# Kernel tuning notes

Measured on AMD Instinct MI355X. Metric: run time of the kernel, lower is better.

Reference implementation:

```python
import jax, jax.numpy as jnp
import numpy as np

B, S, H = 2, 2048, 256
NS, NR = 512, 512
FFN_RATIO = 4


def setup_inputs() -> dict:
    key = jax.random.key(0)
    ks = jax.random.split(key, 8)
    token_reps = jax.random.normal(ks[0], (B, S, H), dtype=jnp.float32)
    token_masks = jnp.ones((B, S), dtype=bool)
    span_reps = jax.random.normal(ks[1], (B, NS, H), dtype=jnp.float32)
    # spans: start in [0, S-16), length in [1, 16) -> valid [start, end) windows
    starts = jax.random.randint(ks[2], (B, NS), 0, S - 16)
    lens = jax.random.randint(ks[3], (B, NS), 1, 16)
    span_ids = jnp.stack([starts, starts + lens], axis=-1)  # (B, NS, 2)
    rel_ids = jax.random.randint(ks[4], (B, NR, 2), 0, NS)  # (B, NR, 2)
    rel_masks = jnp.ones((B, NR), dtype=bool)
    neg_limit = jnp.float32(-6.0e4)
    d_in = 3 * H
    d_ff = FFN_RATIO * d_in
    W1 = jax.random.normal(ks[5], (d_in, d_ff), dtype=jnp.float32) / np.float32(np.sqrt(d_in))
    b1 = jnp.zeros((d_ff,), dtype=jnp.float32)
    W2 = jax.random.normal(ks[6], (d_ff, H), dtype=jnp.float32) / np.float32(np.sqrt(d_ff))
    b2 = jnp.zeros((H,), dtype=jnp.float32)
    return {
        "token_reps": token_reps, "token_masks": token_masks,
        "span_reps": span_reps, "span_ids": span_ids,
        "rel_ids": rel_ids, "rel_masks": rel_masks, "neg_limit": neg_limit,
        "W1": W1, "b1": b1, "W2": W2, "b2": b2,
    }


def reference(token_reps, token_masks, span_reps, span_ids, rel_ids, rel_masks,
              neg_limit, W1, b1, W2, b2):
    seq_len = token_reps.shape[1]
    head_ids = rel_ids[..., 0]  # (B, NR)
    tail_ids = rel_ids[..., 1]
    # gather head/tail span reps: (B, NR, H)
    head_reps = jnp.take_along_axis(span_reps, head_ids[..., None], axis=1)
    tail_reps = jnp.take_along_axis(span_reps, tail_ids[..., None], axis=1)
    # span boundaries per relation: (B, NR)
    head_start = jnp.take_along_axis(span_ids[..., 0], head_ids, axis=1)
    head_end = jnp.take_along_axis(span_ids[..., 1], head_ids, axis=1)
    tail_start = jnp.take_along_axis(span_ids[..., 0], tail_ids, axis=1)
    tail_end = jnp.take_along_axis(span_ids[..., 1], tail_ids, axis=1)
    seq = jnp.arange(seq_len)[None, None, :]  # (1, 1, S)
    head_m = (seq >= head_start[..., None]) & (seq < head_end[..., None])
    tail_m = (seq >= tail_start[..., None]) & (seq < tail_end[..., None])
    # 'between' base context: tokens strictly between the two spans
    lo = jnp.minimum(head_end, tail_end)[..., None]
    hi = jnp.maximum(head_start, tail_start)[..., None]
    base = (seq >= lo) & (seq < hi)
    ctx_mask = base & ~(head_m | tail_m) & rel_masks[..., None] & token_masks[:, None, :]  # (B, NR, S)
    # masked max-pool over seq: (B, NR, S, H) -> (B, NR, H)
    masked = jnp.where(ctx_mask[..., None], token_reps[:, None, :, :], neg_limit)
    context_reps = jnp.max(masked, axis=2)
    # no-context fallback: fully-masked relations -> zero vector
    all_masked = jnp.all(context_reps == neg_limit, axis=-1)
    context_reps = jnp.where(all_masked[..., None], jnp.float32(0.0), context_reps)
    rel_reps = jnp.concatenate([head_reps, tail_reps, context_reps], axis=-1)  # (B, NR, 3H)
    h = jax.nn.relu(rel_reps @ W1 + b1)  # dropout = identity at inference
    return h @ W2 + b2
```

## Files before the change

kernel.cpp:

```cpp
#include <hip/hip_runtime.h>
#include <hip/hip_bf16.h>
#include <stdint.h>

#define Bb 2
#define Ss 2048
#define Hh 256
#define NSs 512
#define NRr 512
#define DIN 768
#define DFF 3072
#define Mm (Bb*NRr)
#define KSLICES 4

typedef __attribute__((ext_vector_type(8))) short short8;
typedef __attribute__((ext_vector_type(4))) short short4b;
typedef __attribute__((ext_vector_type(4))) float floatx4;
typedef __attribute__((ext_vector_type(2))) float floatx2;

__device__ __forceinline__ short f2bf(float f) {
  uint32_t u = __float_as_uint(f);
  u += 0x7fffu + ((u >> 16) & 1u);
  return (short)(u >> 16);
}

__device__ __forceinline__ short4b f2bf4(floatx4 v) {
  short4b r;
  r.x = f2bf(v.x); r.y = f2bf(v.y); r.z = f2bf(v.z); r.w = f2bf(v.w);
  return r;
}

__device__ __forceinline__ uint32_t pack_bf2_rne(float lo, float hi) {
  uint32_t ul = __float_as_uint(lo); ul += 0x7fffu + ((ul >> 16) & 1u);
  uint32_t uh = __float_as_uint(hi); uh += 0x7fffu + ((uh >> 16) & 1u);
  return (uh & 0xffff0000u) | (ul >> 16);
}

__device__ __forceinline__ uint32_t max_packed(uint32_t a, uint32_t b) {
  float a0 = __uint_as_float(a << 16), a1 = __uint_as_float(a & 0xffff0000u);
  float b0 = __uint_as_float(b << 16), b1 = __uint_as_float(b & 0xffff0000u);
  float m0 = fmaxf(a0, b0), m1 = fmaxf(a1, b1);
  return (__float_as_uint(m1) & 0xffff0000u) | (__float_as_uint(m0) >> 16);
}

__device__ __forceinline__ void gld_lds16(const void* g, void* l) {
  __builtin_amdgcn_global_load_lds(
      (const __attribute__((address_space(1))) void*)g,
      (__attribute__((address_space(3))) void*)l, 16, 0, 0);
}

__global__ __launch_bounds__(256) void ctx_lds(
    const float* __restrict__ token_reps,
    const int* __restrict__ span_ids,
    const int* __restrict__ rel_ids,
    short* __restrict__ X)
{
  __shared__ uint32_t Lv[8][Ss];
  int t = threadIdx.x;
  int bid = blockIdx.x;
  int b = bid >> 7;
  int r7 = bid & 127;
  int L = ((r7 >> 6) & 1) * 8 + (r7 & 7);
  int m = (r7 >> 3) & 7;
  int g = L * 8 + m;
  int c2 = g * 2;

#pragma unroll
  for (int j = 0; j < 8; ++j) {
    int i = j * 256 + t;
    floatx2 v = *(const floatx2*)&token_reps[((size_t)b * Ss + i) * Hh + c2];
    Lv[0][i] = pack_bf2_rne(v.x, v.y);
  }
  __syncthreads();
#pragma unroll
  for (int k = 1; k <= 7; ++k) {
    int d = 1 << (k - 1);
#pragma unroll
    for (int j = 0; j < 8; ++j) {
      int i = j * 256 + t;
      Lv[k][i] = max_packed(Lv[k - 1][i], Lv[k - 1][min(i + d, Ss - 1)]);
    }
    __syncthreads();
  }

#pragma unroll
  for (int rr = 0; rr < 2; ++rr) {
    int r = rr * 256 + t;
    int hid = rel_ids[(b * NRr + r) * 2 + 0];
    int tid_ = rel_ids[(b * NRr + r) * 2 + 1];
    int hs = span_ids[(b * NSs + hid) * 2 + 0];
    int he = span_ids[(b * NSs + hid) * 2 + 1];
    int ts = span_ids[(b * NSs + tid_) * 2 + 0];
    int te = span_ids[(b * NSs + tid_) * 2 + 1];
    int lo = min(he, te), hi = max(hs, ts);
    int s1 = hs, e1 = he, s2 = ts, e2 = te;
    if (s2 < s1) { s1 = ts; e1 = te; s2 = hs; e2 = he; }

    int ia[3], ibv[3], ni = 0;
    if (e1 >= s2) {
      int me = max(e1, e2);
      int a = lo, bb2 = min(hi, s1); if (a < bb2) { ia[ni]=a; ibv[ni]=bb2; ni++; }
      a = max(lo, me); bb2 = hi;     if (a < bb2) { ia[ni]=a; ibv[ni]=bb2; ni++; }
    } else {
      int a = lo, bb2 = min(hi, s1);      if (a < bb2) { ia[ni]=a; ibv[ni]=bb2; ni++; }
      a = max(lo, e1); bb2 = min(hi, s2); if (a < bb2) { ia[ni]=a; ibv[ni]=bb2; ni++; }
      a = max(lo, e2); bb2 = hi;          if (a < bb2) { ia[ni]=a; ibv[ni]=bb2; ni++; }
    }

    uint32_t acc = 0xff80ff80u;
    for (int q = 0; q < ni; ++q) {
      int a = ia[q], e = ibv[q], len = e - a;
      if (len >= 128) {
        int x = a;
        for (; x + 128 <= e; x += 128) acc = max_packed(acc, Lv[7][x]);
        if (x < e) acc = max_packed(acc, Lv[7][e - 128]);
      } else {
        int k = 31 - __builtin_clz(len);
        acc = max_packed(acc, Lv[k][a]);
        acc = max_packed(acc, Lv[k][e - (1 << k)]);
      }
    }
    if (ni == 0) acc = 0;
    *(uint32_t*)&X[(size_t)(b * NRr + r) * DIN + 2 * Hh + c2] = acc;
  }
}

__global__ __launch_bounds__(256) void gather_and_convT(
    const float* __restrict__ span_reps,
    const int* __restrict__ rel_ids,
    short* __restrict__ X,
    const float* __restrict__ W1, short* __restrict__ W1t,
    const float* __restrict__ W2, short* __restrict__ W2t)
{
  __shared__ float tile[32][33];
  int bid = blockIdx.x;
  int tid = threadIdx.x;

  if (bid < Mm / 4) {
    int w = tid >> 6, lane = tid & 63;
    int br = bid * 4 + w;
    int b = br >> 9, r = br & (NRr - 1);
    int hid = rel_ids[(b * NRr + r) * 2 + 0];
    int tid_ = rel_ids[(b * NRr + r) * 2 + 1];
    int c4 = lane * 4;
    floatx4 hr = *(const floatx4*)&span_reps[((size_t)b * NSs + hid) * Hh + c4];
    floatx4 tr = *(const floatx4*)&span_reps[((size_t)b * NSs + tid_) * Hh + c4];
    size_t base = (size_t)br * DIN;
    *(short4b*)&X[base + c4]      = f2bf4(hr);
    *(short4b*)&X[base + Hh + c4] = f2bf4(tr);
  } else {
    int cb = bid - Mm / 4;
    const float* W; short* Wt; int K, N, bx, by;
    if (cb < 2304) { W = W1; Wt = W1t; K = DIN; N = DFF; bx = cb % 96; by = cb / 96; }
    else { cb -= 2304; W = W2; Wt = W2t; K = DFF; N = Hh; bx = cb % 8; by = cb / 8; }
    int n0 = bx * 32, k0 = by * 32;
    int tx = tid & 31, ty = tid >> 5;
#pragma unroll
    for (int i = 0; i < 4; ++i)
      tile[ty + i * 8][tx] = W[(size_t)(k0 + ty + i * 8) * N + n0 + tx];
    __syncthreads();
#pragma unroll
    for (int i = 0; i < 4; ++i)
      Wt[(size_t)(n0 + ty + i * 8) * K + k0 + tx] = f2bf(tile[tx][ty + i * 8]);
  }
}

__global__ __launch_bounds__(256) void ctx_kernel(
    const float* __restrict__ token_reps,
    const float* __restrict__ span_reps,
    const int* __restrict__ span_ids,
    const int* __restrict__ rel_ids,
    short* __restrict__ X)
{
  int br = blockIdx.x;
  int b = br >> 9;
  int r = br & (NRr - 1);
  int c = threadIdx.x;
  int hid = rel_ids[(b * NRr + r) * 2 + 0];
  int tid = rel_ids[(b * NRr + r) * 2 + 1];
  int hs = span_ids[(b * NSs + hid) * 2 + 0];
  int he = span_ids[(b * NSs + hid) * 2 + 1];
  int ts = span_ids[(b * NSs + tid) * 2 + 0];
  int te = span_ids[(b * NSs + tid) * 2 + 1];
  int lo = min(he, te);
  int hi = max(hs, ts);
  float m = -3.4e38f;
  bool found = false;
  const float* tr = token_reps + ((size_t)b * Ss) * Hh + c;
  for (int s = lo; s < hi; ++s) {
    bool inspan = (s >= hs && s < he) || (s >= ts && s < te);
    if (!inspan) { found = true; m = fmaxf(m, tr[(size_t)s * Hh]); }
  }
  float ctx = found ? m : 0.0f;
  size_t base = (size_t)br * DIN;
  X[base + c]          = f2bf(span_reps[((size_t)b * NSs + hid) * Hh + c]);
  X[base + Hh + c]     = f2bf(span_reps[((size_t)b * NSs + tid) * Hh + c]);
  X[base + 2 * Hh + c] = f2bf(ctx);
}

__global__ void convT(const float* __restrict__ W, short* __restrict__ Wt,
                      int K, int N) {
  __shared__ float tile[32][33];
  int n0 = blockIdx.x * 32, k0 = blockIdx.y * 32;
  int tx = threadIdx.x, ty = threadIdx.y;
#pragma unroll
  for (int i = 0; i < 4; ++i)
    tile[ty + i * 8][tx] = W[(size_t)(k0 + ty + i * 8) * N + n0 + tx];
  __syncthreads();
#pragma unroll
  for (int i = 0; i < 4; ++i)
    Wt[(size_t)(n0 + ty + i * 8) * K + k0 + tx] = f2bf(tile[tx][ty + i * 8]);
}

template <int BM, int BN, bool RELU_BF16>
__global__ __launch_bounds__(256) void gemm_bt(
    const short* __restrict__ A, const short* __restrict__ Bt,
    const float* __restrict__ bias, void* __restrict__ Cout,
    int M, int N, int K) {
  constexpr int BK = 32;
  constexpr int WM = BM / 2, WN = BN / 2;
  constexpr int MT = WM / 16, NT = WN / 16;
  __shared__ __align__(16) short As[BM * BK];
  __shared__ __align__(16) short Bs[BN * BK];

  int tid = threadIdx.x;
  int lane = tid & 63, w = tid >> 6;
  int wi = w & 1, wj = w >> 1;
  int m0 = blockIdx.x * BM, n0 = blockIdx.y * BN;
  int quad = lane >> 4, l16 = lane & 15;

  floatx4 acc[MT][NT];
#pragma unroll
  for (int i = 0; i < MT; ++i)
#pragma unroll
    for (int j = 0; j < NT; ++j)
      acc[i][j] = (floatx4){0.f, 0.f, 0.f, 0.f};

  constexpr int ACH = BM / 16;
  constexpr int BCH = BN / 16;

  for (int kk = 0; kk < K; kk += BK) {
#pragma unroll
    for (int i = 0; i < ACH / 4; ++i) {
      int chunk = w * (ACH / 4) + i;
      int r = chunk * 16 + (lane >> 2);
      gld_lds16(A + (size_t)(m0 + r) * K + kk + (lane & 3) * 8, &As[chunk * 512]);
    }
#pragma unroll
    for (int i = 0; i < BCH / 4; ++i) {
      int chunk = w * (BCH / 4) + i;
      int r = chunk * 16 + (lane >> 2);
      gld_lds16(Bt + (size_t)(n0 + r) * K + kk + (lane & 3) * 8, &Bs[chunk * 512]);
    }
    __syncthreads();

    short8 a[MT], b[NT];
#pragma unroll
    for (int i = 0; i < MT; ++i)
      a[i] = *(const short8*)&As[(wi * WM + i * 16 + l16) * BK + quad * 8];
#pragma unroll
    for (int j = 0; j < NT; ++j)
      b[j] = *(const short8*)&Bs[(wj * WN + j * 16 + l16) * BK + quad * 8];
#pragma unroll
    for (int i = 0; i < MT; ++i)
#pragma unroll
      for (int j = 0; j < NT; ++j)
        acc[i][j] = __builtin_amdgcn_mfma_f32_16x16x32_bf16(a[i], b[j],
                                                            acc[i][j], 0, 0, 0);
    __syncthreads();
  }

#pragma unroll
  for (int i = 0; i < MT; ++i) {
#pragma unroll
    for (int j = 0; j < NT; ++j) {
      int col = n0 + wj * WN + j * 16 + l16;
      float bv = bias[col];
#pragma unroll
      for (int rr = 0; rr < 4; ++rr) {
        int row = m0 + wi * WM + i * 16 + quad * 4 + rr;
        float v = acc[i][j][rr] + bv;
        if (RELU_BF16) {
          v = fmaxf(v, 0.f);
          ((short*)Cout)[(size_t)row * N + col] = f2bf(v);
        } else {
          ((float*)Cout)[(size_t)row * N + col] = v;
        }
      }
    }
  }
}

__global__ __launch_bounds__(256) void gemm_bt_splitk(
    const short* __restrict__ A, const short* __restrict__ Bt,
    float* __restrict__ P, int M, int N, int K) {
  constexpr int BM = 64, BN = 64, BK = 32;
  constexpr int WM = 32, WN = 32;
  constexpr int MT = 2, NT = 2;
  __shared__ __align__(16) short As[BM * BK];
  __shared__ __align__(16) short Bs[BN * BK];

  int tid = threadIdx.x;
  int lane = tid & 63, w = tid >> 6;
  int wi = w & 1, wj = w >> 1;
  int m0 = blockIdx.x * BM, n0 = blockIdx.y * BN;
  int z = blockIdx.z;
  int ksl = K / KSLICES;
  int k_begin = z * ksl, k_end = k_begin + ksl;
  int quad = lane >> 4, l16 = lane & 15;

  floatx4 acc[MT][NT];
#pragma unroll
  for (int i = 0; i < MT; ++i)
#pragma unroll
    for (int j = 0; j < NT; ++j)
      acc[i][j] = (floatx4){0.f, 0.f, 0.f, 0.f};

  for (int kk = k_begin; kk < k_end; kk += BK) {
    {
      int r = w * 16 + (lane >> 2);
      gld_lds16(A + (size_t)(m0 + r) * K + kk + (lane & 3) * 8, &As[w * 512]);
      gld_lds16(Bt + (size_t)(n0 + r) * K + kk + (lane & 3) * 8, &Bs[w * 512]);
    }
    __syncthreads();

    short8 a[MT], b[NT];
#pragma unroll
    for (int i = 0; i < MT; ++i)
      a[i] = *(const short8*)&As[(wi * WM + i * 16 + l16) * BK + quad * 8];
#pragma unroll
    for (int j = 0; j < NT; ++j)
      b[j] = *(const short8*)&Bs[(wj * WN + j * 16 + l16) * BK + quad * 8];
#pragma unroll
    for (int i = 0; i < MT; ++i)
#pragma unroll
      for (int j = 0; j < NT; ++j)
        acc[i][j] = __builtin_amdgcn_mfma_f32_16x16x32_bf16(a[i], b[j],
                                                            acc[i][j], 0, 0, 0);
    __syncthreads();
  }

  float* Pz = P + (size_t)z * M * N;
#pragma unroll
  for (int i = 0; i < MT; ++i)
#pragma unroll
    for (int j = 0; j < NT; ++j) {
      int col = n0 + wj * WN + j * 16 + l16;
#pragma unroll
      for (int rr = 0; rr < 4; ++rr) {
        int row = m0 + wi * WM + i * 16 + quad * 4 + rr;
        Pz[(size_t)row * N + col] = acc[i][j][rr];
      }
    }
}

__global__ __launch_bounds__(256) void splitk_reduce(
    const float* __restrict__ P, const float* __restrict__ bias,
    float* __restrict__ out) {
  int idx = (blockIdx.x * 256 + threadIdx.x) * 4;
  int col = idx & (Hh - 1);
  floatx4 s = *(const floatx4*)&bias[col];
#pragma unroll
  for (int z = 0; z < KSLICES; ++z)
    s += *(const floatx4*)&P[(size_t)z * Mm * Hh + idx];
  *(floatx4*)&out[idx] = s;
}

extern "C" void kernel_launch(void* const* d_in, const int* in_sizes, int n_in,
                              void* d_out, int out_size, void* d_ws,
                              size_t ws_size, hipStream_t stream) {
  const float*   token_reps  = (const float*)d_in[0];
  const float*   span_reps   = (const float*)d_in[2];
  const int*     span_ids    = (const int*)d_in[3];
  const int*     rel_ids     = (const int*)d_in[4];
  const float*   W1 = (const float*)d_in[7];
  const float*   b1 = (const float*)d_in[8];
  const float*   W2 = (const float*)d_in[9];
  const float*   b2 = (const float*)d_in[10];
  float* out = (float*)d_out;

  char* ws = (char*)d_ws;
  short* X    = (short*)ws;
  short* W1t  = X + (size_t)Mm * DIN;
  short* W2t  = W1t + (size_t)DFF * DIN;
  short* hbuf = W2t + (size_t)Hh * DFF;
  size_t bf16_elems = (size_t)Mm * DIN + (size_t)DFF * DIN +
                      (size_t)Hh * DFF + (size_t)Mm * DFF;
  size_t off = (bf16_elems * sizeof(short) + 255) & ~(size_t)255;
  float* Pbuf = (float*)(ws + off);
  size_t need = off + (size_t)KSLICES * Mm * Hh * sizeof(float);

  bool fast = (ws_size >= need);
  if (fast) {
    hipLaunchKernelGGL(ctx_lds, dim3(256), dim3(256), 0, stream,
                       token_reps, span_ids, rel_ids, X);
    hipLaunchKernelGGL(gather_and_convT, dim3(Mm / 4 + 2304 + 768), dim3(256),
                       0, stream, span_reps, rel_ids, X, W1, W1t, W2, W2t);
  } else {
    hipLaunchKernelGGL(ctx_kernel, dim3(Mm), dim3(256), 0, stream,
                       token_reps, span_reps, span_ids, rel_ids, X);
    hipLaunchKernelGGL(convT, dim3(DFF / 32, DIN / 32), dim3(32, 8), 0, stream,
                       W1, W1t, DIN, DFF);
    hipLaunchKernelGGL(convT, dim3(Hh / 32, DFF / 32), dim3(32, 8), 0, stream,
                       W2, W2t, DFF, Hh);
  }
  hipLaunchKernelGGL((gemm_bt<64, 128, true>), dim3(Mm / 64, DFF / 128),
                     dim3(256), 0, stream, X, W1t, b1, (void*)hbuf, Mm, DFF, DIN);
  if (fast) {
    hipLaunchKernelGGL(gemm_bt_splitk, dim3(Mm / 64, Hh / 64, KSLICES),
                       dim3(256), 0, stream, hbuf, W2t, Pbuf, Mm, Hh, DFF);
    hipLaunchKernelGGL(splitk_reduce, dim3(Mm * Hh / 1024), dim3(256), 0,
                       stream, Pbuf, b2, out);
  } else {
    hipLaunchKernelGGL((gemm_bt<64, 64, false>), dim3(Mm / 64, Hh / 64),
                       dim3(256), 0, stream, hbuf, W2t, b2, (void*)out,
                       Mm, Hh, DFF);
  }
}
```

Measured before the change: 123.1 us.

## Merge prep kernels and replace split-K GEMM2 with in-block warp split-K

Result: faster. 118.4 us (-3.8%).

```diff
diff --git a/kernel.cpp b/kernel.cpp
--- a/kernel.cpp
+++ b/kernel.cpp
@@ -10,7 +10,6 @@
 #define DIN 768
 #define DFF 3072
 #define Mm (Bb*NRr)
-#define KSLICES 4
 
 typedef __attribute__((ext_vector_type(8))) short short8;
 typedef __attribute__((ext_vector_type(4))) short short4b;
@@ -48,96 +47,89 @@
       (__attribute__((address_space(3))) void*)l, 16, 0, 0);
 }
 
-__global__ __launch_bounds__(256) void ctx_lds(
+__global__ __launch_bounds__(256) void prep_all(
     const float* __restrict__ token_reps,
+    const float* __restrict__ span_reps,
     const int* __restrict__ span_ids,
-    const int* __restrict__ rel_ids,
-    short* __restrict__ X)
-{
-  __shared__ uint32_t Lv[8][Ss];
-  int t = threadIdx.x;
-  int bid = blockIdx.x;
-  int b = bid >> 7;
-  int r7 = bid & 127;
-  int L = ((r7 >> 6) & 1) * 8 + (r7 & 7);
-  int m = (r7 >> 3) & 7;
-  int g = L * 8 + m;
-  int c2 = g * 2;
-
-#pragma unroll
-  for (int j = 0; j < 8; ++j) {
-    int i = j * 256 + t;
-    floatx2 v = *(const floatx2*)&token_reps[((size_t)b * Ss + i) * Hh + c2];
-    Lv[0][i] = pack_bf2_rne(v.x, v.y);
-  }
-  __syncthreads();
-#pragma unroll
-  for (int k = 1; k <= 7; ++k) {
-    int d = 1 << (k - 1);
-#pragma unroll
-    for (int j = 0; j < 8; ++j) {
-      int i = j * 256 + t;
-      Lv[k][i] = max_packed(Lv[k - 1][i], Lv[k - 1][min(i + d, Ss - 1)]);
-    }
-    __syncthreads();
-  }
-
-#pragma unroll
-  for (int rr = 0; rr < 2; ++rr) {
-    int r = rr * 256 + t;
-    int hid = rel_ids[(b * NRr + r) * 2 + 0];
-    int tid_ = rel_ids[(b * NRr + r) * 2 + 1];
-    int hs = span_ids[(b * NSs + hid) * 2 + 0];
-    int he = span_ids[(b * NSs + hid) * 2 + 1];
-    int ts = span_ids[(b * NSs + tid_) * 2 + 0];
-    int te = span_ids[(b * NSs + tid_) * 2 + 1];
-    int lo = min(he, te), hi = max(hs, ts);
-    int s1 = hs, e1 = he, s2 = ts, e2 = te;
-    if (s2 < s1) { s1 = ts; e1 = te; s2 = hs; e2 = he; }
-
-    int ia[3], ibv[3], ni = 0;
-    if (e1 >= s2) {
-      int me = max(e1, e2);
-      int a = lo, bb2 = min(hi, s1); if (a < bb2) { ia[ni]=a; ibv[ni]=bb2; ni++; }
-      a = max(lo, me); bb2 = hi;     if (a < bb2) { ia[ni]=a; ibv[ni]=bb2; ni++; }
-    } else {
-      int a = lo, bb2 = min(hi, s1);      if (a < bb2) { ia[ni]=a; ibv[ni]=bb2; ni++; }
-      a = max(lo, e1); bb2 = min(hi, s2); if (a < bb2) { ia[ni]=a; ibv[ni]=bb2; ni++; }
-      a = max(lo, e2); bb2 = hi;          if (a < bb2) { ia[ni]=a; ibv[ni]=bb2; ni++; }
-    }
-
-    uint32_t acc = 0xff80ff80u;
-    for (int q = 0; q < ni; ++q) {
-      int a = ia[q], e = ibv[q], len = e - a;
-      if (len >= 128) {
-        int x = a;
-        for (; x + 128 <= e; x += 128) acc = max_packed(acc, Lv[7][x]);
-        if (x < e) acc = max_packed(acc, Lv[7][e - 128]);
-      } else {
-        int k = 31 - __builtin_clz(len);
-        acc = max_packed(acc, Lv[k][a]);
-        acc = max_packed(acc, Lv[k][e - (1 << k)]);
-      }
-    }
-    if (ni == 0) acc = 0;
-    *(uint32_t*)&X[(size_t)(b * NRr + r) * DIN + 2 * Hh + c2] = acc;
-  }
-}
-
-__global__ __launch_bounds__(256) void gather_and_convT(
-    const float* __restrict__ span_reps,
     const int* __restrict__ rel_ids,
     short* __restrict__ X,
     const float* __restrict__ W1, short* __restrict__ W1t,
     const float* __restrict__ W2, short* __restrict__ W2t)
 {
-  __shared__ float tile[32][33];
+  __shared__ __align__(16) uint32_t LvRaw[8 * Ss];
   int bid = blockIdx.x;
-  int tid = threadIdx.x;
-
-  if (bid < Mm / 4) {
-    int w = tid >> 6, lane = tid & 63;
-    int br = bid * 4 + w;
+  int t = threadIdx.x;
+
+  if (bid < 256) {
+    uint32_t (*Lv)[Ss] = (uint32_t(*)[Ss])LvRaw;
+    int b = bid >> 7;
+    int r7 = bid & 127;
+    int L = ((r7 >> 6) & 1) * 8 + (r7 & 7);
+    int m = (r7 >> 3) & 7;
+    int g = L * 8 + m;
+    int c2 = g * 2;
+
+#pragma unroll
+    for (int j = 0; j < 8; ++j) {
+      int i = j * 256 + t;
+      floatx2 v = *(const floatx2*)&token_reps[((size_t)b * Ss + i) * Hh + c2];
+      Lv[0][i] = pack_bf2_rne(v.x, v.y);
+    }
+    __syncthreads();
+#pragma unroll
+    for (int k = 1; k <= 7; ++k) {
+      int d = 1 << (k - 1);
+#pragma unroll
+      for (int j = 0; j < 8; ++j) {
+        int i = j * 256 + t;
+        Lv[k][i] = max_packed(Lv[k - 1][i], Lv[k - 1][min(i + d, Ss - 1)]);
+      }
+      __syncthreads();
+    }
+
+#pragma unroll
+    for (int rr = 0; rr < 2; ++rr) {
+      int r = rr * 256 + t;
+      int hid = rel_ids[(b * NRr + r) * 2 + 0];
+      int tid_ = rel_ids[(b * NRr + r) * 2 + 1];
+      int hs = span_ids[(b * NSs + hid) * 2 + 0];
+      int he = span_ids[(b * NSs + hid) * 2 + 1];
+      int ts = span_ids[(b * NSs + tid_) * 2 + 0];
+      int te = span_ids[(b * NSs + tid_) * 2 + 1];
+      int lo = min(he, te), hi = max(hs, ts);
+      int s1 = hs, e1 = he, s2 = ts, e2 = te;
+      if (s2 < s1) { s1 = ts; e1 = te; s2 = hs; e2 = he; }
+
+      int ia[3], ibv[3], ni = 0;
+      if (e1 >= s2) {
+        int me = max(e1, e2);
+        int a = lo, bb2 = min(hi, s1); if (a < bb2) { ia[ni]=a; ibv[ni]=bb2; ni++; }
+        a = max(lo, me); bb2 = hi;     if (a < bb2) { ia[ni]=a; ibv[ni]=bb2; ni++; }
+      } else {
+        int a = lo, bb2 = min(hi, s1);      if (a < bb2) { ia[ni]=a; ibv[ni]=bb2; ni++; }
+        a = max(lo, e1); bb2 = min(hi, s2); if (a < bb2) { ia[ni]=a; ibv[ni]=bb2; ni++; }
+        a = max(lo, e2); bb2 = hi;          if (a < bb2) { ia[ni]=a; ibv[ni]=bb2; ni++; }
+      }
+
+      uint32_t acc = 0xff80ff80u;
+      for (int q = 0; q < ni; ++q) {
+        int a = ia[q], e = ibv[q], len = e - a;
+        if (len >= 128) {
+          int x = a;
+          for (; x + 128 <= e; x += 128) acc = max_packed(acc, Lv[7][x]);
+          if (x < e) acc = max_packed(acc, Lv[7][e - 128]);
+        } else {
+          int k = 31 - __builtin_clz(len);
+          acc = max_packed(acc, Lv[k][a]);
+          acc = max_packed(acc, Lv[k][e - (1 << k)]);
+        }
+      }
+      if (ni == 0) acc = 0;
+      *(uint32_t*)&X[(size_t)(b * NRr + r) * DIN + 2 * Hh + c2] = acc;
+    }
+  } else if (bid < 512) {
+    int w = t >> 6, lane = t & 63;
+    int br = (bid - 256) * 4 + w;
     int b = br >> 9, r = br & (NRr - 1);
     int hid = rel_ids[(b * NRr + r) * 2 + 0];
     int tid_ = rel_ids[(b * NRr + r) * 2 + 1];
@@ -148,12 +140,13 @@
     *(short4b*)&X[base + c4]      = f2bf4(hr);
     *(short4b*)&X[base + Hh + c4] = f2bf4(tr);
   } else {
-    int cb = bid - Mm / 4;
+    float (*tile)[33] = (float(*)[33])LvRaw;
+    int cb = bid - 512;
     const float* W; short* Wt; int K, N, bx, by;
     if (cb < 2304) { W = W1; Wt = W1t; K = DIN; N = DFF; bx = cb % 96; by = cb / 96; }
     else { cb -= 2304; W = W2; Wt = W2t; K = DFF; N = Hh; bx = cb % 8; by = cb / 8; }
     int n0 = bx * 32, k0 = by * 32;
-    int tx = tid & 31, ty = tid >> 5;
+    int tx = t & 31, ty = t >> 5;
 #pragma unroll
     for (int i = 0; i < 4; ++i)
       tile[ty + i * 8][tx] = W[(size_t)(k0 + ty + i * 8) * N + n0 + tx];
@@ -162,6 +155,166 @@
     for (int i = 0; i < 4; ++i)
       Wt[(size_t)(n0 + ty + i * 8) * K + k0 + tx] = f2bf(tile[tx][ty + i * 8]);
   }
+}
+
+template <int BM, int BN, bool RELU_BF16>
+__global__ __launch_bounds__(256) void gemm_bt(
+    const short* __restrict__ A, const short* __restrict__ Bt,
+    const float* __restrict__ bias, void* __restrict__ Cout,
+    int M, int N, int K) {
+  constexpr int BK = 32;
+  constexpr int WM = BM / 2, WN = BN / 2;
+  constexpr int MT = WM / 16, NT = WN / 16;
+  __shared__ __align__(16) short As[BM * BK];
+  __shared__ __align__(16) short Bs[BN * BK];
+
+  int tid = threadIdx.x;
+  int lane = tid & 63, w = tid >> 6;
+  int wi = w & 1, wj = w >> 1;
+  int m0 = blockIdx.x * BM, n0 = blockIdx.y * BN;
+  int quad = lane >> 4, l16 = lane & 15;
+
+  floatx4 acc[MT][NT];
+#pragma unroll
+  for (int i = 0; i < MT; ++i)
+#pragma unroll
+    for (int j = 0; j < NT; ++j)
+      acc[i][j] = (floatx4){0.f, 0.f, 0.f, 0.f};
+
+  constexpr int ACH = BM / 16;
+  constexpr int BCH = BN / 16;
+
+  for (int kk = 0; kk < K; kk += BK) {
+#pragma unroll
+    for (int i = 0; i < ACH / 4; ++i) {
+      int chunk = w * (ACH / 4) + i;
+      int r = chunk * 16 + (lane >> 2);
+      gld_lds16(A + (size_t)(m0 + r) * K + kk + (lane & 3) * 8, &As[chunk * 512]);
+    }
+#pragma unroll
+    for (int i = 0; i < BCH / 4; ++i) {
+      int chunk = w * (BCH / 4) + i;
+      int r = chunk * 16 + (lane >> 2);
+      gld_lds16(Bt + (size_t)(n0 + r) * K + kk + (lane & 3) * 8, &Bs[chunk * 512]);
+    }
+    __syncthreads();
+
+    short8 a[MT], b[NT];
+#pragma unroll
+    for (int i = 0; i < MT; ++i)
+      a[i] = *(const short8*)&As[(wi * WM + i * 16 + l16) * BK + quad * 8];
+#pragma unroll
+    for (int j = 0; j < NT; ++j)
+      b[j] = *(const short8*)&Bs[(wj * WN + j * 16 + l16) * BK + quad * 8];
+#pragma unroll
+    for (int i = 0; i < MT; ++i)
+#pragma unroll
+      for (int j = 0; j < NT; ++j)
+        acc[i][j] = __builtin_amdgcn_mfma_f32_16x16x32_bf16(a[i], b[j],
+                                                            acc[i][j], 0, 0, 0);
+    __syncthreads();
+  }
+
+#pragma unroll
+  for (int i = 0; i < MT; ++i) {
+#pragma unroll
+    for (int j = 0; j < NT; ++j) {
+      int col = n0 + wj * WN + j * 16 + l16;
+      float bv = bias[col];
+#pragma unroll
+      for (int rr = 0; rr < 4; ++rr) {
+        int row = m0 + wi * WM + i * 16 + quad * 4 + rr;
+        float v = acc[i][j][rr] + bv;
+        if (RELU_BF16) {
+          v = fmaxf(v, 0.f);
+          ((short*)Cout)[(size_t)row * N + col] = f2bf(v);
+        } else {
+          ((float*)Cout)[(size_t)row * N + col] = v;
+        }
+      }
+    }
+  }
+}
+
+__global__ __launch_bounds__(256) void gemm2_wsk(
+    const short* __restrict__ A,
+    const short* __restrict__ Bt,
+    const float* __restrict__ bias,
+    float* __restrict__ out)
+{
+  constexpr int K = DFF, N = Hh;
+  __shared__ __align__(16) short S[4][2][2][1024];
+  int tid = threadIdx.x, lane = tid & 63, w = tid >> 6;
+  int m0 = (blockIdx.x >> 3) * 32, n0 = (blockIdx.x & 7) * 32;
+  int quad = lane >> 4, l16 = lane & 15;
+  int kb = w * (K / 4);
+  int r = lane >> 2;
+  int co = (lane & 3) * 8;
+
+  floatx4 acc[2][2];
+#pragma unroll
+  for (int i = 0; i < 2; ++i)
+#pragma unroll
+    for (int j = 0; j < 2; ++j)
+      acc[i][j] = (floatx4){0.f, 0.f, 0.f, 0.f};
+
+  {
+    short* As = &S[w][0][0][0];
+    short* Bs = &S[w][0][1][0];
+    gld_lds16(A + (size_t)(m0 + r) * K + kb + co, As);
+    gld_lds16(A + (size_t)(m0 + 16 + r) * K + kb + co, As + 512);
+    gld_lds16(Bt + (size_t)(n0 + r) * K + kb + co, Bs);
+    gld_lds16(Bt + (size_t)(n0 + 16 + r) * K + kb + co, Bs + 512);
+  }
+
+  for (int it = 0; it < 24; ++it) {
+    int buf = it & 1;
+    if (it + 1 < 24) {
+      int kk = kb + (it + 1) * 32;
+      short* As = &S[w][buf ^ 1][0][0];
+      short* Bs = &S[w][buf ^ 1][1][0];
+      gld_lds16(A + (size_t)(m0 + r) * K + kk + co, As);
+      gld_lds16(A + (size_t)(m0 + 16 + r) * K + kk + co, As + 512);
+      gld_lds16(Bt + (size_t)(n0 + r) * K + kk + co, Bs);
+      gld_lds16(Bt + (size_t)(n0 + 16 + r) * K + kk + co, Bs + 512);
+      asm volatile("s_waitcnt vmcnt(4)" ::: "memory");
+    } else {
+      asm volatile("s_waitcnt vmcnt(0)" ::: "memory");
+    }
+    const short* As = &S[w][buf][0][0];
+    const short* Bs = &S[w][buf][1][0];
+    short8 a[2], b[2];
+#pragma unroll
+    for (int i = 0; i < 2; ++i)
+      a[i] = *(const short8*)&As[(i * 16 + l16) * 32 + quad * 8];
+#pragma unroll
+    for (int j = 0; j < 2; ++j)
+      b[j] = *(const short8*)&Bs[(j * 16 + l16) * 32 + quad * 8];
+#pragma unroll
+    for (int i = 0; i < 2; ++i)
+#pragma unroll
+      for (int j = 0; j < 2; ++j)
+        acc[i][j] = __builtin_amdgcn_mfma_f32_16x16x32_bf16(a[i], b[j],
+                                                            acc[i][j], 0, 0, 0);
+  }
+
+  float* red = (float*)&S[w][0][0][0];
+#pragma unroll
+  for (int i = 0; i < 2; ++i)
+#pragma unroll
+    for (int j = 0; j < 2; ++j)
+#pragma unroll
+      for (int rr = 0; rr < 4; ++rr)
+        red[(i * 16 + quad * 4 + rr) * 32 + (j * 16 + l16)] = acc[i][j][rr];
+  __syncthreads();
+
+  int e = tid * 4;
+  int row = e >> 5, col = e & 31;
+  floatx4 s = *(const floatx4*)&bias[n0 + col];
+#pragma unroll
+  for (int w2 = 0; w2 < 4; ++w2)
+    s += *(const floatx4*)&((const float*)&S[w2][0][0][0])[e];
+  *(floatx4*)&out[(size_t)(m0 + row) * N + n0 + col] = s;
 }
 
 __global__ __launch_bounds__(256) void ctx_kernel(
@@ -211,160 +364,6 @@
     Wt[(size_t)(n0 + ty + i * 8) * K + k0 + tx] = f2bf(tile[tx][ty + i * 8]);
 }
 
-template <int BM, int BN, bool RELU_BF16>
-__global__ __launch_bounds__(256) void gemm_bt(
-    const short* __restrict__ A, const short* __restrict__ Bt,
-    const float* __restrict__ bias, void* __restrict__ Cout,
-    int M, int N, int K) {
-  constexpr int BK = 32;
-  constexpr int WM = BM / 2, WN = BN / 2;
-  constexpr int MT = WM / 16, NT = WN / 16;
-  __shared__ __align__(16) short As[BM * BK];
-  __shared__ __align__(16) short Bs[BN * BK];
-
-  int tid = threadIdx.x;
-  int lane = tid & 63, w = tid >> 6;
-  int wi = w & 1, wj = w >> 1;
-  int m0 = blockIdx.x * BM, n0 = blockIdx.y * BN;
-  int quad = lane >> 4, l16 = lane & 15;
-
-  floatx4 acc[MT][NT];
-#pragma unroll
-  for (int i = 0; i < MT; ++i)
-#pragma unroll
-    for (int j = 0; j < NT; ++j)
-      acc[i][j] = (floatx4){0.f, 0.f, 0.f, 0.f};
-
-  constexpr int ACH = BM / 16;
-  constexpr int BCH = BN / 16;
-
-  for (int kk = 0; kk < K; kk += BK) {
-#pragma unroll
-    for (int i = 0; i < ACH / 4; ++i) {
-      int chunk = w * (ACH / 4) + i;
-      int r = chunk * 16 + (lane >> 2);
-      gld_lds16(A + (size_t)(m0 + r) * K + kk + (lane & 3) * 8, &As[chunk * 512]);
-    }
-#pragma unroll
-    for (int i = 0; i < BCH / 4; ++i) {
-      int chunk = w * (BCH / 4) + i;
-      int r = chunk * 16 + (lane >> 2);
-      gld_lds16(Bt + (size_t)(n0 + r) * K + kk + (lane & 3) * 8, &Bs[chunk * 512]);
-    }
-    __syncthreads();
-
-    short8 a[MT], b[NT];
-#pragma unroll
-    for (int i = 0; i < MT; ++i)
-      a[i] = *(const short8*)&As[(wi * WM + i * 16 + l16) * BK + quad * 8];
-#pragma unroll
-    for (int j = 0; j < NT; ++j)
-      b[j] = *(const short8*)&Bs[(wj * WN + j * 16 + l16) * BK + quad * 8];
-#pragma unroll
-    for (int i = 0; i < MT; ++i)
-#pragma unroll
-      for (int j = 0; j < NT; ++j)
-        acc[i][j] = __builtin_amdgcn_mfma_f32_16x16x32_bf16(a[i], b[j],
-                                                            acc[i][j], 0, 0, 0);
-    __syncthreads();
-  }
-
-#pragma unroll
-  for (int i = 0; i < MT; ++i) {
-#pragma unroll
-    for (int j = 0; j < NT; ++j) {
-      int col = n0 + wj * WN + j * 16 + l16;
-      float bv = bias[col];
-#pragma unroll
-      for (int rr = 0; rr < 4; ++rr) {
-        int row = m0 + wi * WM + i * 16 + quad * 4 + rr;
-        float v = acc[i][j][rr] + bv;
-        if (RELU_BF16) {
-          v = fmaxf(v, 0.f);
-          ((short*)Cout)[(size_t)row * N + col] = f2bf(v);
-        } else {
-          ((float*)Cout)[(size_t)row * N + col] = v;
-        }
-      }
-    }
-  }
-}
-
-__global__ __launch_bounds__(256) void gemm_bt_splitk(
-    const short* __restrict__ A, const short* __restrict__ Bt,
-    float* __restrict__ P, int M, int N, int K) {
-  constexpr int BM = 64, BN = 64, BK = 32;
-  constexpr int WM = 32, WN = 32;
-  constexpr int MT = 2, NT = 2;
-  __shared__ __align__(16) short As[BM * BK];
-  __shared__ __align__(16) short Bs[BN * BK];
-
-  int tid = threadIdx.x;
-  int lane = tid & 63, w = tid >> 6;
-  int wi = w & 1, wj = w >> 1;
-  int m0 = blockIdx.x * BM, n0 = blockIdx.y * BN;
-  int z = blockIdx.z;
-  int ksl = K / KSLICES;
-  int k_begin = z * ksl, k_end = k_begin + ksl;
-  int quad = lane >> 4, l16 = lane & 15;
-
-  floatx4 acc[MT][NT];
-#pragma unroll
-  for (int i = 0; i < MT; ++i)
-#pragma unroll
-    for (int j = 0; j < NT; ++j)
-      acc[i][j] = (floatx4){0.f, 0.f, 0.f, 0.f};
-
-  for (int kk = k_begin; kk < k_end; kk += BK) {
-    {
-      int r = w * 16 + (lane >> 2);
-      gld_lds16(A + (size_t)(m0 + r) * K + kk + (lane & 3) * 8, &As[w * 512]);
-      gld_lds16(Bt + (size_t)(n0 + r) * K + kk + (lane & 3) * 8, &Bs[w * 512]);
-    }
-    __syncthreads();
-
-    short8 a[MT], b[NT];
-#pragma unroll
-    for (int i = 0; i < MT; ++i)
-      a[i] = *(const short8*)&As[(wi * WM + i * 16 + l16) * BK + quad * 8];
-#pragma unroll
-    for (int j = 0; j < NT; ++j)
-      b[j] = *(const short8*)&Bs[(wj * WN + j * 16 + l16) * BK + quad * 8];
-#pragma unroll
-    for (int i = 0; i < MT; ++i)
-#pragma unroll
-      for (int j = 0; j < NT; ++j)
-        acc[i][j] = __builtin_amdgcn_mfma_f32_16x16x32_bf16(a[i], b[j],
-                                                            acc[i][j], 0, 0, 0);
-    __syncthreads();
-  }
-
-  float* Pz = P + (size_t)z * M * N;
-#pragma unroll
-  for (int i = 0; i < MT; ++i)
-#pragma unroll
-    for (int j = 0; j < NT; ++j) {
-      int col = n0 + wj * WN + j * 16 + l16;
-#pragma unroll
-      for (int rr = 0; rr < 4; ++rr) {
-        int row = m0 + wi * WM + i * 16 + quad * 4 + rr;
-        Pz[(size_t)row * N + col] = acc[i][j][rr];
-      }
-    }
-}
-
-__global__ __launch_bounds__(256) void splitk_reduce(
-    const float* __restrict__ P, const float* __restrict__ bias,
-    float* __restrict__ out) {
-  int idx = (blockIdx.x * 256 + threadIdx.x) * 4;
-  int col = idx & (Hh - 1);
-  floatx4 s = *(const floatx4*)&bias[col];
-#pragma unroll
-  for (int z = 0; z < KSLICES; ++z)
-    s += *(const floatx4*)&P[(size_t)z * Mm * Hh + idx];
-  *(floatx4*)&out[idx] = s;
-}
-
 extern "C" void kernel_launch(void* const* d_in, const int* in_sizes, int n_in,
                               void* d_out, int out_size, void* d_ws,
                               size_t ws_size, hipStream_t stream) {
@@ -385,16 +384,18 @@
   short* hbuf = W2t + (size_t)Hh * DFF;
   size_t bf16_elems = (size_t)Mm * DIN + (size_t)DFF * DIN +
                       (size_t)Hh * DFF + (size_t)Mm * DFF;
-  size_t off = (bf16_elems * sizeof(short) + 255) & ~(size_t)255;
-  float* Pbuf = (float*)(ws + off);
-  size_t need = off + (size_t)KSLICES * Mm * Hh * sizeof(float);
+  size_t need = bf16_elems * sizeof(short);
 
   bool fast = (ws_size >= need);
   if (fast) {
-    hipLaunchKernelGGL(ctx_lds, dim3(256), dim3(256), 0, stream,
-                       token_reps, span_ids, rel_ids, X);
-    hipLaunchKernelGGL(gather_and_convT, dim3(Mm / 4 + 2304 + 768), dim3(256),
-                       0, stream, span_reps, rel_ids, X, W1, W1t, W2, W2t);
+    hipLaunchKernelGGL(prep_all, dim3(512 + 2304 + 768), dim3(256), 0, stream,
+                       token_reps, span_reps, span_ids, rel_ids, X,
+                       W1, W1t, W2, W2t);
+    hipLaunchKernelGGL((gemm_bt<64, 128, true>), dim3(Mm / 64, DFF / 128),
+                       dim3(256), 0, stream, X, W1t, b1, (void*)hbuf,
+                       Mm, DFF, DIN);
+    hipLaunchKernelGGL(gemm2_wsk, dim3(256), dim3(256), 0, stream,
+                       hbuf, W2t, b2, out);
   } else {
     hipLaunchKernelGGL(ctx_kernel, dim3(Mm), dim3(256), 0, stream,
                        token_reps, span_reps, span_ids, rel_ids, X);
@@ -402,15 +403,9 @@
                        W1, W1t, DIN, DFF);
     hipLaunchKernelGGL(convT, dim3(Hh / 32, DFF / 32), dim3(32, 8), 0, stream,
                        W2, W2t, DFF, Hh);
-  }
-  hipLaunchKernelGGL((gemm_bt<64, 128, true>), dim3(Mm / 64, DFF / 128),
-                     dim3(256), 0, stream, X, W1t, b1, (void*)hbuf, Mm, DFF, DIN);
-  if (fast) {
-    hipLaunchKernelGGL(gemm_bt_splitk, dim3(Mm / 64, Hh / 64, KSLICES),
-                       dim3(256), 0, stream, hbuf, W2t, Pbuf, Mm, Hh, DFF);
-    hipLaunchKernelGGL(splitk_reduce, dim3(Mm * Hh / 1024), dim3(256), 0,
-                       stream, Pbuf, b2, out);
-  } else {
+    hipLaunchKernelGGL((gemm_bt<64, 128, true>), dim3(Mm / 64, DFF / 128),
+                       dim3(256), 0, stream, X, W1t, b1, (void*)hbuf,
+                       Mm, DFF, DIN);
     hipLaunchKernelGGL((gemm_bt<64, 64, false>), dim3(Mm / 64, Hh / 64),
                        dim3(256), 0, stream, hbuf, W2t, b2, (void*)out,
                        Mm, Hh, DFF);
```
